# Kernel optimization log

Measured on AMD Instinct MI355X. Metric: run time of the kernel, lower is better.

The kernel has to match this reference:

```python
import jax, jax.numpy as jnp
import numpy as np

D_MODEL = 1024
NUM_HEADS = 16
D_K = D_MODEL // NUM_HEADS
THETA = 10000.0
B, S = 4, 2048


def _rope(x, theta=THETA):
    # x: [b, n, s, d_k]; interleaved pair rotation with base theta
    d = x.shape[-1]
    s = x.shape[-2]
    inv_freq = theta ** (-jnp.arange(0, d, 2, dtype=jnp.float32) / d)  # [d/2]
    pos = jnp.arange(s, dtype=jnp.float32)
    ang = pos[:, None] * inv_freq[None, :]          # [s, d/2]
    cos, sin = jnp.cos(ang), jnp.sin(ang)           # broadcast over b, n
    x1 = x[..., 0::2]
    x2 = x[..., 1::2]
    r1 = x1 * cos - x2 * sin
    r2 = x1 * sin + x2 * cos
    out = jnp.stack([r1, r2], axis=-1).reshape(x.shape)
    return out.astype(x.dtype)


def setup_inputs() -> dict:
    key = jax.random.key(0)
    ks = jax.random.split(key, 5)
    scale = 1.0 / np.sqrt(D_MODEL)
    return {
        "x": jax.random.normal(ks[0], (B, S, D_MODEL), dtype=jnp.float32),
        "W_q": jax.random.normal(ks[1], (D_MODEL, D_MODEL), dtype=jnp.float32) * scale,
        "W_k": jax.random.normal(ks[2], (D_MODEL, D_MODEL), dtype=jnp.float32) * scale,
        "W_v": jax.random.normal(ks[3], (D_MODEL, D_MODEL), dtype=jnp.float32) * scale,
        "W_o": jax.random.normal(ks[4], (D_MODEL, D_MODEL), dtype=jnp.float32) * scale,
    }


def reference(x, W_q, W_k, W_v, W_o):
    b, s, _ = x.shape
    # QKV projections (Linear stores weight as [out, in]; y = x @ W.T)
    q = jnp.einsum("bsd,ed->bse", x, W_q).reshape(b, s, NUM_HEADS, D_K).transpose(0, 2, 1, 3)
    k = jnp.einsum("bsd,ed->bse", x, W_k).reshape(b, s, NUM_HEADS, D_K).transpose(0, 2, 1, 3)
    v = jnp.einsum("bsd,ed->bse", x, W_v).reshape(b, s, NUM_HEADS, D_K).transpose(0, 2, 1, 3)
    q = _rope(q)
    k = _rope(k)
    scale = 1.0 / jnp.sqrt(jnp.asarray(D_K, dtype=x.dtype))
    scores = jnp.einsum("bnqd,bnkd->bnqk", q, k) * scale  # [b,n,s,s]
    causal = jnp.tril(jnp.ones((s, s), dtype=bool))
    scores = jnp.where(causal, scores, jnp.asarray(-jnp.inf, dtype=scores.dtype))
    attn = jax.nn.softmax(scores, axis=-1)
    out = jnp.einsum("bnqk,bnkd->bnqd", attn, v)          # [b,n,s,d_k]
    out = out.transpose(0, 2, 1, 3).reshape(b, s, D_MODEL)
    return jnp.einsum("bsd,ed->bse", out, W_o)
```

## Files before the change

kernel.cpp:

```cpp
#include <hip/hip_runtime.h>

#define AS1 __attribute__((address_space(1)))
#define AS3 __attribute__((address_space(3)))

typedef short short8 __attribute__((ext_vector_type(8)));
typedef float f32x4 __attribute__((ext_vector_type(4)));

#define DM 1024
#define NH 16
#define DKH 64
#define SEQ 2048
#define NB 4
#define ROWS (NB*SEQ)
#define QTILES (SEQ/128)

__device__ __forceinline__ unsigned short f2bf(float x) {
    union { float f; unsigned u; } v; v.f = x;
    unsigned r = v.u + 0x7fffu + ((v.u >> 16) & 1u);
    return (unsigned short)(r >> 16);
}
__device__ __forceinline__ float bf2f(unsigned short b) {
    union { unsigned u; float f; } v; v.u = ((unsigned)b) << 16;
    return v.f;
}
__device__ __forceinline__ unsigned cvtpk_bf16(float lo, float hi) {
    unsigned r;
    asm("v_cvt_pk_bf16_f32 %0, %1, %2" : "=v"(r) : "v"(lo), "v"(hi));
    return r;
}

__device__ __forceinline__ void gload_lds16(const void* g, void* l) {
    const AS1 unsigned int* gp = (const AS1 unsigned int*)(unsigned long long)g;
    AS3 unsigned int* lp = (AS3 unsigned int*)(unsigned)(unsigned long long)l;
    __builtin_amdgcn_global_load_lds(gp, lp, 16, 0, 0);
}

__device__ __forceinline__ f32x4 mfma_bf16(short8 a, short8 b, f32x4 c) {
    return __builtin_amdgcn_mfma_f32_16x16x32_bf16(a, b, c, 0, 0, 0);
}

__global__ void __launch_bounds__(256) prep_kernel(
    const float* __restrict__ x,
    const float* __restrict__ Wq, const float* __restrict__ Wk,
    const float* __restrict__ Wv, const float* __restrict__ Wo,
    unsigned short* __restrict__ xb, unsigned short* __restrict__ wbase,
    float2* __restrict__ tab) {
    int bid = blockIdx.x, tid = threadIdx.x;
    if (bid < 12288) {
        const float* src;
        unsigned short* dst;
        int i;
        if (bid < 8192) {
            src = x; dst = xb; i = bid * 256 + tid;
        } else {
            int id2 = bid - 8192;
            int w = id2 >> 10;
            src = w == 0 ? Wq : (w == 1 ? Wk : (w == 2 ? Wv : Wo));
            dst = wbase + (size_t)w * (1024 * 1024);
            i = (id2 & 1023) * 256 + tid;
        }
        float4 v = reinterpret_cast<const float4*>(src)[i];
        ushort4 o;
        o.x = f2bf(v.x); o.y = f2bf(v.y); o.z = f2bf(v.z); o.w = f2bf(v.w);
        reinterpret_cast<ushort4*>(dst)[i] = o;
    } else {
        int idx = (bid - 12288) * 256 + tid;
        int pos = idx >> 5, i = idx & 31;
        float inv = powf(10000.0f, -(float)i * (1.0f / 32.0f));
        float ang = (float)pos * inv;
        float2 cs; cs.x = cosf(ang); cs.y = sinf(ang);
        tab[idx] = cs;
    }
}

__global__ void __launch_bounds__(256) transpose_v_kernel(const unsigned short* __restrict__ V,
                                                          unsigned short* __restrict__ Vt) {
    __shared__ unsigned short T[4096];
    const int tid = threadIdx.x;
    const int s0 = blockIdx.x * 64, bh = blockIdx.y;
    const int b = bh >> 4, h = bh & 15;
    const unsigned short* src = V + (size_t)(b * SEQ + s0) * DM + h * 64;
    #pragma unroll
    for (int i = 0; i < 2; ++i) {
        int r = i * 32 + (tid >> 3), cg = tid & 7;
        short8 v = *(const short8*)(src + (size_t)r * DM + cg * 8);
        *(short8*)(T + r * 64 + ((cg ^ (r >> 3)) << 3)) = v;
    }
    __syncthreads();
    unsigned short* dst = Vt + (size_t)bh * 64 * SEQ + s0;
    #pragma unroll
    for (int i = 0; i < 2; ++i) {
        int d = i * 32 + (tid >> 3), kg = tid & 7;
        int kc = kg >> 2, m = kg & 3;
        short8 o;
        #pragma unroll
        for (int jj = 0; jj < 8; ++jj) {
            int t = 32 * kc + 16 * (jj >> 2) + 4 * m + (jj & 3);
            o[jj] = (short)T[t * 64 + (((d >> 3) ^ (t >> 3)) << 3) + (d & 7)];
        }
        *(short8*)(dst + (size_t)d * SEQ + kg * 8) = o;
    }
}

template <int STORE_F32>
__device__ __forceinline__ void gemm_bt_body(const unsigned short* __restrict__ A,
                                             const unsigned short* __restrict__ Bw,
                                             void* __restrict__ C, int m0, int n0,
                                             const float2* __restrict__ tab, int rope) {
    __shared__ unsigned short S[128 * 128];
    unsigned short* As = S;
    unsigned short* Bs = S + 128 * 64;
    const int tid = threadIdx.x;
    const int lane = tid & 63;
    const int wave = tid >> 6;
    const int wr = wave >> 1, wc = wave & 1;
    const int l15 = lane & 15, l4 = lane >> 4;

    f32x4 acc[4][4];
    #pragma unroll
    for (int m = 0; m < 4; ++m)
        #pragma unroll
        for (int n = 0; n < 4; ++n) { f32x4 z = {0.f, 0.f, 0.f, 0.f}; acc[m][n] = z; }

    const int srow = wave * 8 + (lane >> 3);
    const int gsw = (lane & 7) ^ (srow & 7);
    const unsigned short* Ag = A + (size_t)m0 * DM;
    const unsigned short* Bg = Bw + (size_t)n0 * DM;

    for (int kt = 0; kt < DM; kt += 64) {
        __syncthreads();
        #pragma unroll
        for (int it = 0; it < 4; ++it) {
            int row = it * 32 + srow;
            gload_lds16(Ag + (size_t)row * DM + kt + gsw * 8, (char*)As + (it * 4 + wave) * 1024);
            gload_lds16(Bg + (size_t)row * DM + kt + gsw * 8, (char*)Bs + (it * 4 + wave) * 1024);
        }
        __syncthreads();
        #pragma unroll
        for (int kc = 0; kc < 2; ++kc) {
            short8 af[4], bfr[4];
            #pragma unroll
            for (int m = 0; m < 4; ++m) {
                int row = 64 * wr + 16 * m + l15;
                int off = row * 128 + (((4 * kc + l4) ^ (row & 7)) << 4);
                af[m] = *(const short8*)((const char*)As + off);
            }
            #pragma unroll
            for (int n = 0; n < 4; ++n) {
                int row = 64 * wc + 16 * n + l15;
                int off = row * 128 + (((4 * kc + l4) ^ (row & 7)) << 4);
                bfr[n] = *(const short8*)((const char*)Bs + off);
            }
            #pragma unroll
            for (int m = 0; m < 4; ++m)
                #pragma unroll
                for (int n = 0; n < 4; ++n)
                    acc[m][n] = mfma_bf16(af[m], bfr[n], acc[m][n]);
        }
    }

    if (STORE_F32) {
        int rbase = m0 + 64 * wr + 4 * l4;
        int cbase = n0 + 64 * wc + l15;
        #pragma unroll
        for (int m = 0; m < 4; ++m)
            #pragma unroll
            for (int n = 0; n < 4; ++n) {
                int c = cbase + 16 * n;
                #pragma unroll
                for (int j = 0; j < 4; ++j)
                    ((float*)C)[(size_t)(rbase + 16 * m + j) * DM + c] = acc[m][n][j];
            }
    } else {
        __syncthreads();
        #pragma unroll
        for (int m = 0; m < 4; ++m) {
            int rb = 64 * wr + 16 * m + 4 * l4;
            int xr = ((rb >> 2) & 7) << 3;
            #pragma unroll
            for (int n = 0; n < 4; ++n) {
                int c = (64 * wc + 16 * n + l15) ^ xr;
                #pragma unroll
                for (int j = 0; j < 4; ++j)
                    S[(rb + j) * 128 + c] = f2bf(acc[m][n][j]);
            }
        }
        __syncthreads();
        unsigned short* Cg = (unsigned short*)C + (size_t)m0 * DM + n0;
        #pragma unroll
        for (int r8 = 0; r8 < 8; ++r8) {
            int row = r8 * 16 + (tid >> 4);
            int oc = tid & 15;
            short8 v = *(const short8*)(S + row * 128 + ((oc ^ ((row >> 2) & 7)) << 3));
            if (rope) {
                int pos = (m0 + row) & (SEQ - 1);
                const float2* tp = tab + pos * 32 + (oc & 7) * 4;
                short8 o;
                #pragma unroll
                for (int tt = 0; tt < 4; ++tt) {
                    float cc = tp[tt].x, ss = tp[tt].y;
                    float e0 = bf2f((unsigned short)v[2 * tt]);
                    float e1 = bf2f((unsigned short)v[2 * tt + 1]);
                    o[2 * tt]     = (short)f2bf(e0 * cc - e1 * ss);
                    o[2 * tt + 1] = (short)f2bf(e0 * ss + e1 * cc);
                }
                v = o;
            }
            *(short8*)(Cg + (size_t)row * DM + oc * 8) = v;
        }
    }
}

__global__ void __launch_bounds__(256) gemm_qkv_kernel(
    const unsigned short* __restrict__ X,
    const unsigned short* __restrict__ Wq, const unsigned short* __restrict__ Wk,
    const unsigned short* __restrict__ Wv,
    unsigned short* __restrict__ Qo, unsigned short* __restrict__ Ko, unsigned short* __restrict__ Vo,
    const float2* __restrict__ tab) {
    int mt = blockIdx.x >> 3, nt = blockIdx.x & 7;
    int z = blockIdx.z;
    const unsigned short* W = z == 0 ? Wq : (z == 1 ? Wk : Wv);
    unsigned short* O = z == 0 ? Qo : (z == 1 ? Ko : Vo);
    gemm_bt_body<0>(X, W, O, mt * 128, nt * 128, tab, z < 2);
}

__global__ void __launch_bounds__(256) gemm_out_kernel(
    const unsigned short* __restrict__ AO, const unsigned short* __restrict__ Wo,
    float* __restrict__ out) {
    int mt = blockIdx.x >> 3, nt = blockIdx.x & 7;
    gemm_bt_body<1>(AO, Wo, out, mt * 128, nt * 128, nullptr, 0);
}

template <int MODE>
__device__ __forceinline__ void attn_tile(const char* bK, const char* bV,
                                          const short8 (&aq)[2][2], f32x4 (&oacc)[2][4],
                                          float (&lrow)[2],
                                          int l15, int l4, int qloc) {
    const float CS = 0.125f * 1.44269504088896f;
    f32x4 sac[2][4];
    #pragma unroll
    for (int f = 0; f < 2; ++f)
        #pragma unroll
        for (int n = 0; n < 4; ++n) { f32x4 z = {0.f, 0.f, 0.f, 0.f}; sac[f][n] = z; }

    #pragma unroll
    for (int kc = 0; kc < 2; ++kc)
        #pragma unroll
        for (int n = 0; n < 4; ++n) {
            int row = 16 * n + l15;
            short8 ak = *(const short8*)(bK + row * 128 + (((4 * kc + l4) ^ (row & 7)) << 4));
            if (MODE < 2) sac[0][n] = mfma_bf16(ak, aq[0][kc], sac[0][n]);
            sac[1][n] = mfma_bf16(ak, aq[1][kc], sac[1][n]);
        }

    short8 pb[2][2];
    #pragma unroll
    for (int f = (MODE == 2 ? 1 : 0); f < 2; ++f) {
        const bool dg = (MODE == 1 && f == 0) || (MODE == 2);
        float pj[4][4];
        float sum = 0.f;
        #pragma unroll
        for (int n = 0; n < 4; ++n)
            #pragma unroll
            for (int j = 0; j < 4; ++j) {
                float s = sac[f][n][j] * CS;
                if (dg && (16 * n + 4 * l4 + j) > qloc) s = -1e30f;
                float p = exp2f(s);
                pj[n][j] = p; sum += p;
            }
        sum += __shfl_xor(sum, 16, 64);
        sum += __shfl_xor(sum, 32, 64);
        lrow[f] += sum;
        #pragma unroll
        for (int kc = 0; kc < 2; ++kc) {
            union { unsigned u[4]; short8 s8; } P;
            P.u[0] = cvtpk_bf16(pj[2 * kc][0], pj[2 * kc][1]);
            P.u[1] = cvtpk_bf16(pj[2 * kc][2], pj[2 * kc][3]);
            P.u[2] = cvtpk_bf16(pj[2 * kc + 1][0], pj[2 * kc + 1][1]);
            P.u[3] = cvtpk_bf16(pj[2 * kc + 1][2], pj[2 * kc + 1][3]);
            pb[f][kc] = P.s8;
        }
    }

    #pragma unroll
    for (int kc = 0; kc < 2; ++kc)
        #pragma unroll
        for (int n = 0; n < 4; ++n) {
            int row = 16 * n + l15;
            short8 av = *(const short8*)(bV + row * 128 + (((4 * kc + l4) ^ (row & 7)) << 4));
            if (MODE < 2) oacc[0][n] = mfma_bf16(av, pb[0][kc], oacc[0][n]);
            oacc[1][n] = mfma_bf16(av, pb[1][kc], oacc[1][n]);
        }
}

__device__ __forceinline__ void attn_one(const unsigned short* __restrict__ Qb,
                                         const unsigned short* __restrict__ Kb,
                                         const unsigned short* __restrict__ Vg,
                                         unsigned short* __restrict__ Ob,
                                         unsigned short* smem, int qt,
                                         int tid, int lane, int wave, int l15, int l4) {
    __syncthreads();

    const int q0 = qt * 128;
    const int qloc = 16 * wave + l15;
    const int NT = 2 * qt + 2;

    short8 aq[2][2];
    #pragma unroll
    for (int f = 0; f < 2; ++f) {
        const unsigned short* p = Qb + (size_t)(q0 + 64 * f + 16 * wave + l15) * DM + 8 * l4;
        aq[f][0] = *(const short8*)p;
        aq[f][1] = *(const short8*)(p + 32);
    }
    asm volatile("s_waitcnt vmcnt(0)" ::: "memory");

    f32x4 oacc[2][4];
    #pragma unroll
    for (int f = 0; f < 2; ++f)
        #pragma unroll
        for (int n = 0; n < 4; ++n) { f32x4 z = {0.f, 0.f, 0.f, 0.f}; oacc[f][n] = z; }
    float lrow[2] = {0.f, 0.f};

    const int srow = wave * 8 + (lane >> 3);
    const int gsw = (lane & 7) ^ (srow & 7);
    const unsigned short* kp = Kb + (size_t)srow * DM + gsw * 8;
    const unsigned short* vp = Vg + (size_t)srow * SEQ + gsw * 8;
    char* LD = (char*)smem;

    {
        char* db = LD;
        gload_lds16(kp, db + wave * 1024);
        gload_lds16(kp + 32 * DM, db + 4096 + wave * 1024);
        gload_lds16(vp, db + 8192 + wave * 1024);
        gload_lds16(vp + 32 * SEQ, db + 12288 + wave * 1024);
        kp += 64 * DM; vp += 64;
    }

    for (int t = 0; t < NT; ++t) {
        const char* bK = LD + (t & 1) * 16384;
        const char* bV = bK + 8192;
        if (t + 1 < NT) {
            char* db = LD + ((t + 1) & 1) * 16384;
            gload_lds16(kp, db + wave * 1024);
            gload_lds16(kp + 32 * DM, db + 4096 + wave * 1024);
            gload_lds16(vp, db + 8192 + wave * 1024);
            gload_lds16(vp + 32 * SEQ, db + 12288 + wave * 1024);
            kp += 64 * DM; vp += 64;
            asm volatile("s_waitcnt vmcnt(4)" ::: "memory");
        } else {
            asm volatile("s_waitcnt vmcnt(0)" ::: "memory");
        }
        __builtin_amdgcn_s_barrier();
        if (t < NT - 2)       attn_tile<0>(bK, bV, aq, oacc, lrow, l15, l4, qloc);
        else if (t == NT - 2) attn_tile<1>(bK, bV, aq, oacc, lrow, l15, l4, qloc);
        else                  attn_tile<2>(bK, bV, aq, oacc, lrow, l15, l4, qloc);
        asm volatile("s_waitcnt lgkmcnt(0)" ::: "memory");
        __builtin_amdgcn_s_barrier();
    }

    unsigned short* ep = smem + wave * 2304;
    float inv[2] = {1.f / lrow[0], 1.f / lrow[1]};
    #pragma unroll
    for (int f = 0; f < 2; ++f)
        #pragma unroll
        for (int n = 0; n < 4; ++n)
            #pragma unroll
            for (int j = 0; j < 4; ++j)
                ep[(f * 16 + l15) * 72 + 16 * n + 4 * l4 + j] = f2bf(oacc[f][n][j] * inv[f]);
    __syncthreads();
    #pragma unroll
    for (int i = 0; i < 4; ++i) {
        int r = i * 8 + (lane >> 3), cg = lane & 7;
        int grow = q0 + 64 * (r >> 4) + 16 * wave + (r & 15);
        *(short8*)(Ob + (size_t)grow * DM + cg * 8) = *(const short8*)(ep + r * 72 + cg * 8);
    }
}

__global__ void __launch_bounds__(256) attn_kernel(const unsigned short* __restrict__ Q,
                                                   const unsigned short* __restrict__ K,
                                                   const unsigned short* __restrict__ Vtg,
                                                   unsigned short* __restrict__ O) {
    __shared__ unsigned short smem[16384];

    const int tid = threadIdx.x, lane = tid & 63, wave = tid >> 6;
    const int l15 = lane & 15, l4 = lane >> 4;
    const int bh = blockIdx.x;
    const int pp = blockIdx.y;
    const int b = bh >> 4, h = bh & 15;
    const size_t base = (size_t)b * SEQ * DM + (size_t)h * DKH;
    const unsigned short* Qb = Q + base;
    const unsigned short* Kb = K + base;
    const unsigned short* Vg = Vtg + (size_t)bh * 64 * SEQ;
    unsigned short* Ob = O + base;

    attn_one(Qb, Kb, Vg, Ob, smem, QTILES - 1 - pp, tid, lane, wave, l15, l4);
    attn_one(Qb, Kb, Vg, Ob, smem, pp, tid, lane, wave, l15, l4);
}

extern "C" void kernel_launch(void* const* d_in, const int* in_sizes, int n_in,
                              void* d_out, int out_size, void* d_ws, size_t ws_size,
                              hipStream_t stream) {
    (void)in_sizes; (void)n_in; (void)out_size; (void)ws_size;
    const float* x  = (const float*)d_in[0];
    const float* Wq = (const float*)d_in[1];
    const float* Wk = (const float*)d_in[2];
    const float* Wv = (const float*)d_in[3];
    const float* Wo = (const float*)d_in[4];
    float* out = (float*)d_out;

    char* ws = (char*)d_ws;
    const size_t MB = 1024 * 1024;
    unsigned short* xb  = (unsigned short*)(ws);
    unsigned short* Vtg = (unsigned short*)(ws);
    unsigned short* wqb = (unsigned short*)(ws + 16 * MB);
    unsigned short* wkb = (unsigned short*)(ws + 18 * MB);
    unsigned short* wvb = (unsigned short*)(ws + 20 * MB);
    unsigned short* wob = (unsigned short*)(ws + 22 * MB);
    unsigned short* Qb  = (unsigned short*)(ws + 24 * MB);
    unsigned short* Kb  = (unsigned short*)(ws + 40 * MB);
    unsigned short* Vb  = (unsigned short*)(ws + 56 * MB);
    unsigned short* AO  = (unsigned short*)(ws + 72 * MB);
    float2* tab = (float2*)(ws + 88 * MB);

    prep_kernel<<<12544, 256, 0, stream>>>(x, Wq, Wk, Wv, Wo, xb, wqb, tab);
    gemm_qkv_kernel<<<dim3(512, 1, 3), 256, 0, stream>>>(xb, wqb, wkb, wvb, Qb, Kb, Vb, tab);
    transpose_v_kernel<<<dim3(SEQ / 64, NB * NH), 256, 0, stream>>>(Vb, Vtg);
    attn_kernel<<<dim3(NB * NH, QTILES / 2), 256, 0, stream>>>(Qb, Kb, Vtg, AO);
    gemm_out_kernel<<<512, 256, 0, stream>>>(AO, wob, out);
}
```

Measured before the change: 200.5 us.

## Fuse V transpose into QKV GEMM epilogue, fold softmax scale into Q, split attention grid

The V projection epilogue now writes V directly in the transposed per-head layout from shared memory, which removes the separate transpose kernel and its extra read and write of V. The softmax scale times log2(e) is folded into the Q RoPE cos/sin multipliers, so the attention inner loop drops one multiply per score. The attention launch changes from one block handling a paired long and short q-tile to one block per q-tile, with a remapped y-order meant to balance causal work across the schedule. The trade-offs are extra bf16 rounding on the pre-scaled Q, strided scattered writes in the V epilogue, and twice as many attention blocks, each paying its own setup.

```diff
diff --git a/kernel.cpp b/kernel.cpp
--- a/kernel.cpp
+++ b/kernel.cpp
@@ -73,40 +73,12 @@
     }
 }
 
-__global__ void __launch_bounds__(256) transpose_v_kernel(const unsigned short* __restrict__ V,
-                                                          unsigned short* __restrict__ Vt) {
-    __shared__ unsigned short T[4096];
-    const int tid = threadIdx.x;
-    const int s0 = blockIdx.x * 64, bh = blockIdx.y;
-    const int b = bh >> 4, h = bh & 15;
-    const unsigned short* src = V + (size_t)(b * SEQ + s0) * DM + h * 64;
-    #pragma unroll
-    for (int i = 0; i < 2; ++i) {
-        int r = i * 32 + (tid >> 3), cg = tid & 7;
-        short8 v = *(const short8*)(src + (size_t)r * DM + cg * 8);
-        *(short8*)(T + r * 64 + ((cg ^ (r >> 3)) << 3)) = v;
-    }
-    __syncthreads();
-    unsigned short* dst = Vt + (size_t)bh * 64 * SEQ + s0;
-    #pragma unroll
-    for (int i = 0; i < 2; ++i) {
-        int d = i * 32 + (tid >> 3), kg = tid & 7;
-        int kc = kg >> 2, m = kg & 3;
-        short8 o;
-        #pragma unroll
-        for (int jj = 0; jj < 8; ++jj) {
-            int t = 32 * kc + 16 * (jj >> 2) + 4 * m + (jj & 3);
-            o[jj] = (short)T[t * 64 + (((d >> 3) ^ (t >> 3)) << 3) + (d & 7)];
-        }
-        *(short8*)(dst + (size_t)d * SEQ + kg * 8) = o;
-    }
-}
-
 template <int STORE_F32>
 __device__ __forceinline__ void gemm_bt_body(const unsigned short* __restrict__ A,
                                              const unsigned short* __restrict__ Bw,
                                              void* __restrict__ C, int m0, int n0,
-                                             const float2* __restrict__ tab, int rope) {
+                                             const float2* __restrict__ tab, float rs,
+                                             unsigned short* __restrict__ vt, int outmode) {
     __shared__ unsigned short S[128 * 128];
     unsigned short* As = S;
     unsigned short* Bs = S + 128 * 64;
@@ -186,27 +158,50 @@
             }
         }
         __syncthreads();
-        unsigned short* Cg = (unsigned short*)C + (size_t)m0 * DM + n0;
-        #pragma unroll
-        for (int r8 = 0; r8 < 8; ++r8) {
-            int row = r8 * 16 + (tid >> 4);
-            int oc = tid & 15;
-            short8 v = *(const short8*)(S + row * 128 + ((oc ^ ((row >> 2) & 7)) << 3));
-            if (rope) {
-                int pos = (m0 + row) & (SEQ - 1);
-                const float2* tp = tab + pos * 32 + (oc & 7) * 4;
+        if (outmode == 2) {
+            int bidx = m0 >> 11;
+            int stile = m0 & (SEQ - 1);
+            int hA = n0 >> 6;
+            unsigned short* vtb = vt + (size_t)(bidx * (NH * 64) + hA * 64) * SEQ;
+            #pragma unroll
+            for (int rep = 0; rep < 8; ++rep) {
+                int idx = rep * 256 + tid;
+                int vtrow = idx >> 4;
+                int grp = idx & 15;
+                int tg = grp >> 3, kg = grp & 7;
+                int kc = kg >> 2, mq = kg & 3;
                 short8 o;
                 #pragma unroll
-                for (int tt = 0; tt < 4; ++tt) {
-                    float cc = tp[tt].x, ss = tp[tt].y;
-                    float e0 = bf2f((unsigned short)v[2 * tt]);
-                    float e1 = bf2f((unsigned short)v[2 * tt + 1]);
-                    o[2 * tt]     = (short)f2bf(e0 * cc - e1 * ss);
-                    o[2 * tt + 1] = (short)f2bf(e0 * ss + e1 * cc);
+                for (int jj = 0; jj < 8; ++jj) {
+                    int t = 32 * kc + 16 * (jj >> 2) + 4 * mq + (jj & 3);
+                    int r = tg * 64 + t;
+                    o[jj] = (short)S[r * 128 + (vtrow ^ (((r >> 2) & 7) << 3))];
                 }
-                v = o;
-            }
-            *(short8*)(Cg + (size_t)row * DM + oc * 8) = v;
+                *(short8*)(vtb + (size_t)vtrow * SEQ + stile + tg * 64 + kg * 8) = o;
+            }
+        } else {
+            unsigned short* Cg = (unsigned short*)C + (size_t)m0 * DM + n0;
+            #pragma unroll
+            for (int r8 = 0; r8 < 8; ++r8) {
+                int row = r8 * 16 + (tid >> 4);
+                int oc = tid & 15;
+                short8 v = *(const short8*)(S + row * 128 + ((oc ^ ((row >> 2) & 7)) << 3));
+                if (rs > 0.f) {
+                    int pos = (m0 + row) & (SEQ - 1);
+                    const float2* tp = tab + pos * 32 + (oc & 7) * 4;
+                    short8 o;
+                    #pragma unroll
+                    for (int tt = 0; tt < 4; ++tt) {
+                        float cc = tp[tt].x * rs, ss = tp[tt].y * rs;
+                        float e0 = bf2f((unsigned short)v[2 * tt]);
+                        float e1 = bf2f((unsigned short)v[2 * tt + 1]);
+                        o[2 * tt]     = (short)f2bf(e0 * cc - e1 * ss);
+                        o[2 * tt + 1] = (short)f2bf(e0 * ss + e1 * cc);
+                    }
+                    v = o;
+                }
+                *(short8*)(Cg + (size_t)row * DM + oc * 8) = v;
+            }
         }
     }
 }
@@ -215,20 +210,23 @@
     const unsigned short* __restrict__ X,
     const unsigned short* __restrict__ Wq, const unsigned short* __restrict__ Wk,
     const unsigned short* __restrict__ Wv,
-    unsigned short* __restrict__ Qo, unsigned short* __restrict__ Ko, unsigned short* __restrict__ Vo,
+    unsigned short* __restrict__ Qo, unsigned short* __restrict__ Ko,
+    unsigned short* __restrict__ Vtg,
     const float2* __restrict__ tab) {
+    const float CS = 0.125f * 1.44269504088896f;
     int mt = blockIdx.x >> 3, nt = blockIdx.x & 7;
     int z = blockIdx.z;
     const unsigned short* W = z == 0 ? Wq : (z == 1 ? Wk : Wv);
-    unsigned short* O = z == 0 ? Qo : (z == 1 ? Ko : Vo);
-    gemm_bt_body<0>(X, W, O, mt * 128, nt * 128, tab, z < 2);
+    unsigned short* O = z == 0 ? Qo : Ko;
+    gemm_bt_body<0>(X, W, O, mt * 128, nt * 128, tab,
+                    z == 0 ? CS : (z == 1 ? 1.0f : 0.f), Vtg, z == 2 ? 2 : 0);
 }
 
 __global__ void __launch_bounds__(256) gemm_out_kernel(
     const unsigned short* __restrict__ AO, const unsigned short* __restrict__ Wo,
     float* __restrict__ out) {
     int mt = blockIdx.x >> 3, nt = blockIdx.x & 7;
-    gemm_bt_body<1>(AO, Wo, out, mt * 128, nt * 128, nullptr, 0);
+    gemm_bt_body<1>(AO, Wo, out, mt * 128, nt * 128, nullptr, 0.f, nullptr, 0);
 }
 
 template <int MODE>
@@ -236,7 +234,6 @@
                                           const short8 (&aq)[2][2], f32x4 (&oacc)[2][4],
                                           float (&lrow)[2],
                                           int l15, int l4, int qloc) {
-    const float CS = 0.125f * 1.44269504088896f;
     f32x4 sac[2][4];
     #pragma unroll
     for (int f = 0; f < 2; ++f)
@@ -263,7 +260,7 @@
         for (int n = 0; n < 4; ++n)
             #pragma unroll
             for (int j = 0; j < 4; ++j) {
-                float s = sac[f][n][j] * CS;
+                float s = sac[f][n][j];
                 if (dg && (16 * n + 4 * l4 + j) > qloc) s = -1e30f;
                 float p = exp2f(s);
                 pj[n][j] = p; sum += p;
@@ -293,13 +290,23 @@
         }
 }
 
-__device__ __forceinline__ void attn_one(const unsigned short* __restrict__ Qb,
-                                         const unsigned short* __restrict__ Kb,
-                                         const unsigned short* __restrict__ Vg,
-                                         unsigned short* __restrict__ Ob,
-                                         unsigned short* smem, int qt,
-                                         int tid, int lane, int wave, int l15, int l4) {
-    __syncthreads();
+__global__ void __launch_bounds__(256) attn_kernel(const unsigned short* __restrict__ Q,
+                                                   const unsigned short* __restrict__ K,
+                                                   const unsigned short* __restrict__ Vtg,
+                                                   unsigned short* __restrict__ O) {
+    __shared__ unsigned short smem[16384];
+
+    const int tid = threadIdx.x, lane = tid & 63, wave = tid >> 6;
+    const int l15 = lane & 15, l4 = lane >> 4;
+    const int bh = blockIdx.x;
+    const int yg = blockIdx.y >> 2, yl = blockIdx.y & 3;
+    const int qt = yg == 0 ? 15 - yl : (yg == 1 ? yl : (yg == 2 ? 11 - yl : 4 + yl));
+    const int b = bh >> 4, h = bh & 15;
+    const size_t base = (size_t)b * SEQ * DM + (size_t)h * DKH;
+    const unsigned short* Qb = Q + base;
+    const unsigned short* Kb = K + base;
+    const unsigned short* Vg = Vtg + (size_t)bh * 64 * SEQ;
+    unsigned short* Ob = O + base;
 
     const int q0 = qt * 128;
     const int qloc = 16 * wave + l15;
@@ -376,27 +383,6 @@
     }
 }
 
-__global__ void __launch_bounds__(256) attn_kernel(const unsigned short* __restrict__ Q,
-                                                   const unsigned short* __restrict__ K,
-                                                   const unsigned short* __restrict__ Vtg,
-                                                   unsigned short* __restrict__ O) {
-    __shared__ unsigned short smem[16384];
-
-    const int tid = threadIdx.x, lane = tid & 63, wave = tid >> 6;
-    const int l15 = lane & 15, l4 = lane >> 4;
-    const int bh = blockIdx.x;
-    const int pp = blockIdx.y;
-    const int b = bh >> 4, h = bh & 15;
-    const size_t base = (size_t)b * SEQ * DM + (size_t)h * DKH;
-    const unsigned short* Qb = Q + base;
-    const unsigned short* Kb = K + base;
-    const unsigned short* Vg = Vtg + (size_t)bh * 64 * SEQ;
-    unsigned short* Ob = O + base;
-
-    attn_one(Qb, Kb, Vg, Ob, smem, QTILES - 1 - pp, tid, lane, wave, l15, l4);
-    attn_one(Qb, Kb, Vg, Ob, smem, pp, tid, lane, wave, l15, l4);
-}
-
 extern "C" void kernel_launch(void* const* d_in, const int* in_sizes, int n_in,
                               void* d_out, int out_size, void* d_ws, size_t ws_size,
                               hipStream_t stream) {
@@ -411,20 +397,18 @@
     char* ws = (char*)d_ws;
     const size_t MB = 1024 * 1024;
     unsigned short* xb  = (unsigned short*)(ws);
-    unsigned short* Vtg = (unsigned short*)(ws);
     unsigned short* wqb = (unsigned short*)(ws + 16 * MB);
     unsigned short* wkb = (unsigned short*)(ws + 18 * MB);
     unsigned short* wvb = (unsigned short*)(ws + 20 * MB);
     unsigned short* wob = (unsigned short*)(ws + 22 * MB);
     unsigned short* Qb  = (unsigned short*)(ws + 24 * MB);
     unsigned short* Kb  = (unsigned short*)(ws + 40 * MB);
-    unsigned short* Vb  = (unsigned short*)(ws + 56 * MB);
+    unsigned short* Vtg = (unsigned short*)(ws + 56 * MB);
     unsigned short* AO  = (unsigned short*)(ws + 72 * MB);
     float2* tab = (float2*)(ws + 88 * MB);
 
     prep_kernel<<<12544, 256, 0, stream>>>(x, Wq, Wk, Wv, Wo, xb, wqb, tab);
-    gemm_qkv_kernel<<<dim3(512, 1, 3), 256, 0, stream>>>(xb, wqb, wkb, wvb, Qb, Kb, Vb, tab);
-    transpose_v_kernel<<<dim3(SEQ / 64, NB * NH), 256, 0, stream>>>(Vb, Vtg);
-    attn_kernel<<<dim3(NB * NH, QTILES / 2), 256, 0, stream>>>(Qb, Kb, Vtg, AO);
+    gemm_qkv_kernel<<<dim3(512, 1, 3), 256, 0, stream>>>(xb, wqb, wkb, wvb, Qb, Kb, Vtg, tab);
+    attn_kernel<<<dim3(NB * NH, QTILES), 256, 0, stream>>>(Qb, Kb, Vtg, AO);
     gemm_out_kernel<<<512, 256, 0, stream>>>(AO, wob, out);
 }
```

Measured after the change: 183.4 us. 8.5% less time.
